# Kernel tuning notes

Hardware: AMD Instinct MI355X
Metric: run time of the kernel (lower is better)

## Reference

```python
import jax, jax.numpy as jnp
import numpy as np

LN_EPS = 1e-5


def setup_inputs() -> dict:
    key = jax.random.key(0)
    ks = jax.random.split(key, 9)
    B, S, D = 8, 2048, 512
    scale = 1.0 / np.sqrt(D)
    inp = {
        "z_q": jax.random.normal(ks[0], (B, S, D), jnp.float32),
        "z_k": jax.random.normal(ks[1], (B, S, D), jnp.float32),
        "z_v": jax.random.normal(ks[2], (B, S, D), jnp.float32),
        "Wq": jax.random.normal(ks[3], (D, D), jnp.float32) * scale,
        "bq": jnp.zeros((D,), jnp.float32),
        "Wk": jax.random.normal(ks[4], (D, D), jnp.float32) * scale,
        "bk": jnp.zeros((D,), jnp.float32),
        "Wv": jax.random.normal(ks[5], (D, D), jnp.float32) * scale,
        "bv": jnp.zeros((D,), jnp.float32),
        "ln_gamma": jnp.ones((D,), jnp.float32),
        "ln_beta": jnp.zeros((D,), jnp.float32),
    }
    return inp


def reference(z_q, z_k, z_v, Wq, bq, Wk, bk, Wv, bv, ln_gamma, ln_beta):
    # Linear projections (torch Linear: x @ W^T + b)
    Q = jnp.einsum("bsd,ed->bse", z_q, Wq) + bq  # [B, Sq, D]
    K = jnp.einsum("bsd,ed->bse", z_k, Wk) + bk  # [B, Sk, D]
    V = jnp.einsum("bsd,ed->bse", z_v, Wv) + bv  # [B, Sk, D]

    d = K.shape[-1]
    scores = jnp.einsum("bqd,bkd->bqk", Q, K) / jnp.sqrt(jnp.float32(d))
    attn = jax.nn.softmax(scores, axis=-1)  # [B, Sq, Sk]
    z_fused = jnp.einsum("bqk,bkd->bqd", attn, V)

    # LayerNorm over last dim
    mu = jnp.mean(z_fused, axis=-1, keepdims=True)
    var = jnp.var(z_fused, axis=-1, keepdims=True)
    z_norm = (z_fused - mu) * jax.lax.rsqrt(var + LN_EPS)
    return z_norm * ln_gamma + ln_beta
```

## Files before the change

kernel.cpp:

```cpp
#include <hip/hip_runtime.h>

typedef short v8s __attribute__((ext_vector_type(8)));
typedef float v4f __attribute__((ext_vector_type(4)));
typedef unsigned short u16;

#define SCALE_QK 0.04419417382415922f
#define ATTN_LDS (131072 + 17408 + 8192 + 256)

static __device__ __forceinline__ u16 f2bf(float f){
  unsigned u = __float_as_uint(f);
  u += 0x7fffu + ((u >> 16) & 1u);
  return (u16)(u >> 16);
}

static __device__ __forceinline__ void gload16(const void* g, void* l){
  __builtin_amdgcn_global_load_lds(
      (const __attribute__((address_space(1))) unsigned int*)(g),
      (__attribute__((address_space(3))) unsigned int*)(l), 16, 0, 0);
}

static __device__ __forceinline__ void bar_pub(){
  asm volatile("s_waitcnt lgkmcnt(0)" ::: "memory");
  __builtin_amdgcn_s_barrier();
  asm volatile("" ::: "memory");
}

template<int WA, int WB, int RF, int CF>
static __device__ __forceinline__ void proj_body(
    const float* __restrict__ A, const float* __restrict__ Bm,
    const float* __restrict__ bias, bool biasA, float oscale,
    u16* __restrict__ O, size_t ldo, int a0, int b0, char* sm)
{
  constexpr int AR = WA*RF*16;
  constexpr int BR = WB*CF*16;
  char* SA = sm;
  char* SB = sm + AR*64;
  const int t = threadIdx.x;
  const int l = t & 63, lm = l & 15, lg = l >> 4;
  const int w = t >> 6;
  const int wa = w / WB, wb = w % WB;
  const int swz = (lm & 3) << 4;

  v4f acc[RF][CF];
  #pragma unroll
  for (int i=0;i<RF;i++)
    #pragma unroll
    for (int j=0;j<CF;j++) acc[i][j] = (v4f){0.f,0.f,0.f,0.f};

  const int quad = t & 3;
  for (int kt=0; kt<16; ++kt){
    __syncthreads();
    #pragma unroll
    for (int rr0 = 0; rr0 < AR; rr0 += 128){
      int rr = rr0 + (t >> 2);
      const float* g = A + (size_t)(a0+rr)*512 + kt*32 + quad*8;
      float4 x0 = *(const float4*)g;
      float4 x1 = *(const float4*)(g+4);
      int4 pk;
      pk.x = (int)((unsigned)f2bf(x0.x) | ((unsigned)f2bf(x0.y)<<16));
      pk.y = (int)((unsigned)f2bf(x0.z) | ((unsigned)f2bf(x0.w)<<16));
      pk.z = (int)((unsigned)f2bf(x1.x) | ((unsigned)f2bf(x1.y)<<16));
      pk.w = (int)((unsigned)f2bf(x1.z) | ((unsigned)f2bf(x1.w)<<16));
      *(int4*)(SA + rr*64 + ((quad*16) ^ ((rr&3)<<4))) = pk;
    }
    #pragma unroll
    for (int rr0 = 0; rr0 < BR; rr0 += 128){
      int rr = rr0 + (t >> 2);
      const float* g = Bm + (size_t)(b0+rr)*512 + kt*32 + quad*8;
      float4 x0 = *(const float4*)g;
      float4 x1 = *(const float4*)(g+4);
      int4 pk;
      pk.x = (int)((unsigned)f2bf(x0.x) | ((unsigned)f2bf(x0.y)<<16));
      pk.y = (int)((unsigned)f2bf(x0.z) | ((unsigned)f2bf(x0.w)<<16));
      pk.z = (int)((unsigned)f2bf(x1.x) | ((unsigned)f2bf(x1.y)<<16));
      pk.w = (int)((unsigned)f2bf(x1.z) | ((unsigned)f2bf(x1.w)<<16));
      *(int4*)(SB + rr*64 + ((quad*16) ^ ((rr&3)<<4))) = pk;
    }
    __syncthreads();
    v8s af[RF], bf[CF];
    #pragma unroll
    for (int mf=0; mf<RF; ++mf)
      af[mf] = *(const v8s*)(SA + (wa*RF*16 + mf*16 + lm)*64 + ((lg*16) ^ swz));
    #pragma unroll
    for (int nf=0; nf<CF; ++nf)
      bf[nf] = *(const v8s*)(SB + (wb*CF*16 + nf*16 + lm)*64 + ((lg*16) ^ swz));
    #pragma unroll
    for (int mf=0; mf<RF; ++mf)
      #pragma unroll
      for (int nf=0; nf<CF; ++nf)
        acc[mf][nf] = __builtin_amdgcn_mfma_f32_16x16x32_bf16(af[mf], bf[nf], acc[mf][nf], 0, 0, 0);
  }

  float bb[CF];
  if (!biasA){
    #pragma unroll
    for (int nf=0;nf<CF;nf++) bb[nf] = bias[b0 + wb*CF*16 + nf*16 + lm];
  }
  #pragma unroll
  for (int mf=0; mf<RF; ++mf){
    #pragma unroll
    for (int r=0;r<4;r++){
      int ar = a0 + wa*RF*16 + mf*16 + lg*4 + r;
      float ba = biasA ? bias[ar] : 0.0f;
      #pragma unroll
      for (int nf=0;nf<CF;nf++){
        int bc = b0 + wb*CF*16 + nf*16 + lm;
        float v = acc[mf][nf][r] + (biasA ? ba : bb[nf]);
        O[(size_t)ar*ldo + bc] = f2bf(v * oscale);
      }
    }
  }
}

__global__ __launch_bounds__(512, 2) void proj_kernel(
    const float* __restrict__ zq, const float* __restrict__ zk, const float* __restrict__ zv,
    const float* __restrict__ Wq, const float* __restrict__ Wk, const float* __restrict__ Wv,
    const float* __restrict__ bq, const float* __restrict__ bk, const float* __restrict__ bv,
    u16* __restrict__ Qb, u16* __restrict__ Kb, u16* __restrict__ VTb)
{
  extern __shared__ char sm[];
  const int z = blockIdx.y, bx = blockIdx.x;
  if (z == 0)      proj_body<2,4,4,8>(zq, Wq, bq, false, SCALE_QK, Qb, 512, bx*128, 0, sm);
  else if (z == 1) proj_body<2,4,4,8>(zk, Wk, bk, false, 1.0f,     Kb, 512, bx*128, 0, sm);
  else             proj_body<4,2,8,4>(Wv, zv, bv, true,  1.0f,     VTb, 16384, 0, bx*128, sm);
}

static __device__ __forceinline__ void stage_k(const u16* Kb0, int j, char* Kbuf, int w, int l){
  const u16* Kt = Kb0 + (size_t)j*64*512;
  #pragma unroll
  for (int c=0;c<8;c++){
    int r = w*8 + c;
    gload16(Kt + (size_t)r*512 + (((l*16) ^ (c<<4))>>1), Kbuf + r*1024);
  }
}
static __device__ __forceinline__ void stage_v(const u16* Vb0, int j, char* Vbuf, int w, int l){
  const u16* Vt = Vb0 + (size_t)j*64;
  #pragma unroll
  for (int c=0;c<8;c++){
    int e0 = w*64 + c*8;
    gload16(Vt + (size_t)(e0 + (l>>3))*16384 + ((((l&7)*16) ^ ((l>>3)<<4))>>1), Vbuf + e0*128);
  }
}

__global__ __launch_bounds__(512, 2) void attn_kernel(
    const u16* __restrict__ Qg, const u16* __restrict__ Kg, const u16* __restrict__ VTg,
    const float* __restrict__ gamma, const float* __restrict__ beta,
    float* __restrict__ Outg)
{
  extern __shared__ char lds[];
  char*  Kbuf = lds;
  char*  Vbuf = lds + 65536;
  float* Ss   = (float*)(lds + 131072);
  char*  Pb   = lds + 131072 + 17408;
  float* st_l = (float*)(lds + 131072 + 17408 + 8192);

  const int t = threadIdx.x;
  const int l = t & 63;
  const int lm = l & 15, lg = l >> 4;
  const int w = t >> 6;
  const int wm = w >> 2;
  const int wn = w & 3;
  const int bid = blockIdx.x;
  const int b = bid & 7;
  const int q0 = (bid >> 3) * 64;

  const u16* Qt  = Qg  + ((size_t)b*2048 + q0)*512;
  const u16* Kb0 = Kg  + (size_t)b*2048*512;
  const u16* Vb0 = VTg + (size_t)b*2048;

  v8s qf[2][16];
  #pragma unroll
  for (int mf=0; mf<2; ++mf){
    const u16* qp = Qt + (size_t)(wm*32+mf*16+lm)*512 + lg*8;
    #pragma unroll
    for (int st=0; st<16; ++st)
      qf[mf][st] = *(const v8s*)(qp + st*32);
  }

  if (t < 64) st_l[t] = 0.0f;

  v4f acc[2][8];
  #pragma unroll
  for (int i=0;i<2;i++)
    #pragma unroll
    for (int j=0;j<8;j++) acc[i][j] = (v4f){0.f,0.f,0.f,0.f};

  stage_k(Kb0, 0, Kbuf, w, l);
  asm volatile("s_waitcnt vmcnt(0)" ::: "memory");
  bar_pub();
  stage_v(Vb0, 0, Vbuf, w, l);

  #pragma unroll 1
  for (int kt=0; kt<32; ++kt){
    {
      v4f s0 = (v4f){0.f,0.f,0.f,0.f}, s1 = (v4f){0.f,0.f,0.f,0.f};
      const char* kb = Kbuf + (wn*16+lm)*1024;
      const int ksw = (lm&7)<<4;
      #pragma unroll
      for (int st=0; st<16; ++st){
        v8s bfr = *(const v8s*)(kb + ((st*64 + lg*16) ^ ksw));
        s0 = __builtin_amdgcn_mfma_f32_16x16x32_bf16(qf[0][st], bfr, s0, 0,0,0);
        s1 = __builtin_amdgcn_mfma_f32_16x16x32_bf16(qf[1][st], bfr, s1, 0,0,0);
      }
      #pragma unroll
      for (int r=0;r<4;r++){
        Ss[(wm*32 +      lg*4 + r)*68 + wn*16 + lm] = s0[r];
        Ss[(wm*32 + 16 + lg*4 + r)*68 + wn*16 + lm] = s1[r];
      }
    }
    bar_pub();
    if (kt < 31) stage_k(Kb0, kt+1, Kbuf, w, l);
    {
      const int row = t >> 3, sub = t & 7;
      const float* sp = Ss + row*68 + sub*8;
      float4 sa = *(const float4*)sp;
      float4 sb = *(const float4*)(sp+4);
      float p0=__expf(sa.x), p1=__expf(sa.y), p2=__expf(sa.z), p3=__expf(sa.w);
      float p4=__expf(sb.x), p5=__expf(sb.y), p6=__expf(sb.z), p7=__expf(sb.w);
      float ps = ((p0+p1)+(p2+p3))+((p4+p5)+(p6+p7));
      ps += __shfl_xor(ps,1);
      ps += __shfl_xor(ps,2);
      ps += __shfl_xor(ps,4);
      int4 pk;
      pk.x = (int)((unsigned)f2bf(p0) | ((unsigned)f2bf(p1)<<16));
      pk.y = (int)((unsigned)f2bf(p2) | ((unsigned)f2bf(p3)<<16));
      pk.z = (int)((unsigned)f2bf(p4) | ((unsigned)f2bf(p5)<<16));
      pk.w = (int)((unsigned)f2bf(p6) | ((unsigned)f2bf(p7)<<16));
      *(int4*)(Pb + row*128 + ((sub*16) ^ ((row&7)<<4))) = pk;
      if (sub == 0) st_l[row] += ps;
    }
    if (kt < 31) { asm volatile("s_waitcnt vmcnt(8)" ::: "memory"); }
    else         { asm volatile("s_waitcnt vmcnt(0)" ::: "memory"); }
    bar_pub();
    #pragma unroll
    for (int ks=0; ks<2; ++ks){
      const int k2 = ks*64 + lg*16;
      const int psw = (lm&7)<<4;
      v8s pa0 = *(const v8s*)(Pb + (wm*32      + lm)*128 + (k2 ^ psw));
      v8s pa1 = *(const v8s*)(Pb + (wm*32 + 16 + lm)*128 + (k2 ^ psw));
      #pragma unroll
      for (int nf=0; nf<8; ++nf){
        const int e = wn*128 + nf*16 + lm;
        v8s vb = *(const v8s*)(Vbuf + e*128 + (k2 ^ psw));
        acc[0][nf] = __builtin_amdgcn_mfma_f32_16x16x32_bf16(pa0, vb, acc[0][nf], 0,0,0);
        acc[1][nf] = __builtin_amdgcn_mfma_f32_16x16x32_bf16(pa1, vb, acc[1][nf], 0,0,0);
      }
    }
    asm volatile("s_waitcnt vmcnt(0)" ::: "memory");
    bar_pub();
    if (kt < 31) stage_v(Vb0, kt+1, Vbuf, w, l);
  }

  float gv[8], bw[8];
  #pragma unroll
  for (int nf=0;nf<8;nf++){ int col = wn*128+nf*16+lm; gv[nf]=gamma[col]; bw[nf]=beta[col]; }

  float* part = Ss;
  #pragma unroll
  for (int mf=0; mf<2; ++mf){
    #pragma unroll
    for (int r=0;r<4;r++){
      int row = wm*32 + mf*16 + lg*4 + r;
      float inv = 1.0f / st_l[row];
      float s1 = 0.f, s2 = 0.f;
      #pragma unroll
      for (int nf=0;nf<8;nf++){
        float x = acc[mf][nf][r] * inv;
        acc[mf][nf][r] = x;
        s1 += x; s2 += x*x;
      }
      s1 += __shfl_xor(s1,1); s2 += __shfl_xor(s2,1);
      s1 += __shfl_xor(s1,2); s2 += __shfl_xor(s2,2);
      s1 += __shfl_xor(s1,4); s2 += __shfl_xor(s2,4);
      s1 += __shfl_xor(s1,8); s2 += __shfl_xor(s2,8);
      if (lm == 0){
        part[row*4 + wn] = s1;
        part[256 + row*4 + wn] = s2;
      }
    }
  }
  bar_pub();
  float* st_mu = (float*)Pb;
  float* st_rs = (float*)(Pb + 256);
  if (t < 64){
    float s1 = part[t*4+0]+part[t*4+1]+part[t*4+2]+part[t*4+3];
    float s2 = part[256+t*4+0]+part[256+t*4+1]+part[256+t*4+2]+part[256+t*4+3];
    float mu = s1 * (1.0f/512.0f);
    float var = s2 * (1.0f/512.0f) - mu*mu;
    st_mu[t] = mu;
    st_rs[t] = rsqrtf(fmaxf(var, 0.0f) + 1e-5f);
  }
  bar_pub();
  float* Og = Outg + ((size_t)b*2048 + q0)*512;
  #pragma unroll
  for (int mf=0; mf<2; ++mf){
    #pragma unroll
    for (int r=0;r<4;r++){
      int row = wm*32 + mf*16 + lg*4 + r;
      float mu = st_mu[row], rs = st_rs[row];
      #pragma unroll
      for (int nf=0;nf<8;nf++){
        int col = wn*128 + nf*16 + lm;
        Og[(size_t)row*512 + col] = (acc[mf][nf][r] - mu)*rs*gv[nf] + bw[nf];
      }
    }
  }
}

extern "C" void kernel_launch(void* const* d_in, const int* in_sizes, int n_in,
                              void* d_out, int out_size, void* d_ws, size_t ws_size,
                              hipStream_t stream) {
  const float* z_q  = (const float*)d_in[0];
  const float* z_k  = (const float*)d_in[1];
  const float* z_v  = (const float*)d_in[2];
  const float* Wq   = (const float*)d_in[3];
  const float* bq   = (const float*)d_in[4];
  const float* Wk   = (const float*)d_in[5];
  const float* bk   = (const float*)d_in[6];
  const float* Wv   = (const float*)d_in[7];
  const float* bv   = (const float*)d_in[8];
  const float* gam  = (const float*)d_in[9];
  const float* bet  = (const float*)d_in[10];
  float* out = (float*)d_out;

  u16* Qb  = (u16*)d_ws;
  u16* Kb  = Qb + (size_t)16384*512;
  u16* VTb = Kb + (size_t)16384*512;

  hipFuncSetAttribute(reinterpret_cast<const void*>(&proj_kernel),
                      hipFuncAttributeMaxDynamicSharedMemorySize, 40960);
  hipFuncSetAttribute(reinterpret_cast<const void*>(&attn_kernel),
                      hipFuncAttributeMaxDynamicSharedMemorySize, ATTN_LDS);

  proj_kernel<<<dim3(128,3), 512, 40960, stream>>>(z_q, z_k, z_v, Wq, Wk, Wv, bq, bk, bv, Qb, Kb, VTb);
  attn_kernel<<<256, 512, ATTN_LDS, stream>>>(Qb, Kb, VTb, gam, bet, out);
}
```

Baseline: 461.2 us.

## Restructure attention warp tiling, double-buffer K, pre-convert weights to bf16

Weights are converted to bf16 once by a new kernel and then streamed into LDS with async global-to-LDS loads, and the projection is split into separate Q/K and V kernels. The attention kernel is retiled so that each warp owns a slice of the output columns. It double-buffers K tiles in LDS and loads V fragments straight from global memory into registers instead of staging them in LDS. The exp/rowsum is computed directly on the MFMA score registers, which removes the fp32 score scratch and one barrier per iteration. The risks are higher register pressure and uncoalesced V reads from global memory, plus an extra kernel launch.

```diff
diff --git a/kernel.cpp b/kernel.cpp
--- a/kernel.cpp
+++ b/kernel.cpp
@@ -5,124 +5,185 @@
 typedef unsigned short u16;
 
 #define SCALE_QK 0.04419417382415922f
-#define ATTN_LDS (131072 + 17408 + 8192 + 256)
+#define ATTN_LDS 145664
 
 static __device__ __forceinline__ u16 f2bf(float f){
   unsigned u = __float_as_uint(f);
   u += 0x7fffu + ((u >> 16) & 1u);
   return (u16)(u >> 16);
 }
-
+static __device__ __forceinline__ unsigned pk2(float a, float b){
+  return (unsigned)f2bf(a) | ((unsigned)f2bf(b) << 16);
+}
 static __device__ __forceinline__ void gload16(const void* g, void* l){
   __builtin_amdgcn_global_load_lds(
       (const __attribute__((address_space(1))) unsigned int*)(g),
       (__attribute__((address_space(3))) unsigned int*)(l), 16, 0, 0);
 }
-
-static __device__ __forceinline__ void bar_pub(){
+static __device__ __forceinline__ void bar_ds(){
   asm volatile("s_waitcnt lgkmcnt(0)" ::: "memory");
   __builtin_amdgcn_s_barrier();
   asm volatile("" ::: "memory");
 }
 
-template<int WA, int WB, int RF, int CF>
-static __device__ __forceinline__ void proj_body(
-    const float* __restrict__ A, const float* __restrict__ Bm,
-    const float* __restrict__ bias, bool biasA, float oscale,
-    u16* __restrict__ O, size_t ldo, int a0, int b0, char* sm)
+__global__ __launch_bounds__(256) void convert_w(
+    const float* __restrict__ Wq, const float* __restrict__ Wk,
+    const float* __restrict__ Wv, u16* __restrict__ Wo)
 {
-  constexpr int AR = WA*RF*16;
-  constexpr int BR = WB*CF*16;
-  char* SA = sm;
-  char* SB = sm + AR*64;
-  const int t = threadIdx.x;
-  const int l = t & 63, lm = l & 15, lg = l >> 4;
-  const int w = t >> 6;
-  const int wa = w / WB, wb = w % WB;
-  const int swz = (lm & 3) << 4;
-
-  v4f acc[RF][CF];
-  #pragma unroll
-  for (int i=0;i<RF;i++)
-    #pragma unroll
-    for (int j=0;j<CF;j++) acc[i][j] = (v4f){0.f,0.f,0.f,0.f};
-
-  const int quad = t & 3;
+  const float* src = (blockIdx.y==0) ? Wq : (blockIdx.y==1) ? Wk : Wv;
+  u16* dst = Wo + (size_t)blockIdx.y * 262144;
+  int i = blockIdx.x*256 + threadIdx.x;
+  const float4* s = (const float4*)src + (size_t)i*2;
+  float4 a = s[0], b = s[1];
+  *(ushort4*)(dst + (size_t)i*8)     = make_ushort4(f2bf(a.x),f2bf(a.y),f2bf(a.z),f2bf(a.w));
+  *(ushort4*)(dst + (size_t)i*8 + 4) = make_ushort4(f2bf(b.x),f2bf(b.y),f2bf(b.z),f2bf(b.w));
+}
+
+__global__ __launch_bounds__(512, 2) void proj_qk(
+    const float* __restrict__ zq, const float* __restrict__ zk,
+    const u16* __restrict__ Wb,
+    const float* __restrict__ bq, const float* __restrict__ bk,
+    u16* __restrict__ Qb, u16* __restrict__ Kb)
+{
+  __shared__ char SA[128*64];
+  __shared__ char SB[512*64];
+  const int y = blockIdx.y;
+  const float* Z    = y ? zk : zq;
+  const u16*  W     = Wb + (size_t)y*262144;
+  const float* bias = y ? bk : bq;
+  u16* O            = y ? Kb : Qb;
+  const float oscale = y ? 1.0f : SCALE_QK;
+
+  const int t = threadIdx.x, l = t&63, lm = l&15, lg = l>>4, w = t>>6;
+  const int wa = w>>2, wb2 = w&3;
+  const int m0 = blockIdx.x*128;
+
+  v4f acc[4][8];
+  #pragma unroll
+  for (int i=0;i<4;i++)
+    #pragma unroll
+    for (int j=0;j<8;j++) acc[i][j] = (v4f){0.f,0.f,0.f,0.f};
+
+  const int arow = t>>2, aq = t&3;
+  #pragma unroll 1
   for (int kt=0; kt<16; ++kt){
     __syncthreads();
-    #pragma unroll
-    for (int rr0 = 0; rr0 < AR; rr0 += 128){
-      int rr = rr0 + (t >> 2);
-      const float* g = A + (size_t)(a0+rr)*512 + kt*32 + quad*8;
+    {
+      const float* g = Z + (size_t)(m0+arow)*512 + kt*32 + aq*8;
       float4 x0 = *(const float4*)g;
       float4 x1 = *(const float4*)(g+4);
-      int4 pk;
-      pk.x = (int)((unsigned)f2bf(x0.x) | ((unsigned)f2bf(x0.y)<<16));
-      pk.y = (int)((unsigned)f2bf(x0.z) | ((unsigned)f2bf(x0.w)<<16));
-      pk.z = (int)((unsigned)f2bf(x1.x) | ((unsigned)f2bf(x1.y)<<16));
-      pk.w = (int)((unsigned)f2bf(x1.z) | ((unsigned)f2bf(x1.w)<<16));
-      *(int4*)(SA + rr*64 + ((quad*16) ^ ((rr&3)<<4))) = pk;
-    }
-    #pragma unroll
-    for (int rr0 = 0; rr0 < BR; rr0 += 128){
-      int rr = rr0 + (t >> 2);
-      const float* g = Bm + (size_t)(b0+rr)*512 + kt*32 + quad*8;
+      int4 pk = { (int)pk2(x0.x,x0.y), (int)pk2(x0.z,x0.w),
+                  (int)pk2(x1.x,x1.y), (int)pk2(x1.z,x1.w) };
+      *(int4*)(SA + arow*64 + ((aq*16) ^ ((arow&3)<<4))) = pk;
+    }
+    #pragma unroll
+    for (int i=0;i<4;i++){
+      int rbase = i*128 + w*16;
+      int r = rbase + (l>>2), c = l&3;
+      gload16(W + (size_t)r*512 + kt*32 + ((c ^ (r&3))*8), SB + rbase*64);
+    }
+    __syncthreads();
+    v8s af[4], bf[8];
+    #pragma unroll
+    for (int mf=0; mf<4; ++mf){
+      int m = wa*64 + mf*16 + lm;
+      af[mf] = *(const v8s*)(SA + m*64 + ((lg*16) ^ ((m&3)<<4)));
+    }
+    #pragma unroll
+    for (int nf=0; nf<8; ++nf){
+      int n = wb2*128 + nf*16 + lm;
+      bf[nf] = *(const v8s*)(SB + n*64 + ((lg*16) ^ ((n&3)<<4)));
+    }
+    #pragma unroll
+    for (int mf=0; mf<4; ++mf)
+      #pragma unroll
+      for (int nf=0; nf<8; ++nf)
+        acc[mf][nf] = __builtin_amdgcn_mfma_f32_16x16x32_bf16(af[mf], bf[nf], acc[mf][nf], 0,0,0);
+  }
+
+  float bb[8];
+  #pragma unroll
+  for (int nf=0;nf<8;nf++) bb[nf] = bias[wb2*128 + nf*16 + lm];
+  #pragma unroll
+  for (int mf=0; mf<4; ++mf){
+    #pragma unroll
+    for (int r=0;r<4;r++){
+      int m = m0 + wa*64 + mf*16 + lg*4 + r;
+      #pragma unroll
+      for (int nf=0;nf<8;nf++){
+        int n = wb2*128 + nf*16 + lm;
+        O[(size_t)m*512 + n] = f2bf((acc[mf][nf][r] + bb[nf]) * oscale);
+      }
+    }
+  }
+}
+
+__global__ __launch_bounds__(512, 2) void proj_v(
+    const float* __restrict__ zv, const u16* __restrict__ Wvb,
+    const float* __restrict__ bv, u16* __restrict__ VTb)
+{
+  __shared__ char SA[512*64];
+  __shared__ char SB[128*64];
+  const int t = threadIdx.x, l = t&63, lm = l&15, lg = l>>4, w = t>>6;
+  const int wn = w>>1, wm2 = w&1;
+  const int m0 = blockIdx.x*128;
+
+  v4f acc[8][4];
+  #pragma unroll
+  for (int i=0;i<8;i++)
+    #pragma unroll
+    for (int j=0;j<4;j++) acc[i][j] = (v4f){0.f,0.f,0.f,0.f};
+
+  const int brow = t>>2, bq2 = t&3;
+  #pragma unroll 1
+  for (int kt=0; kt<16; ++kt){
+    __syncthreads();
+    {
+      const float* g = zv + (size_t)(m0+brow)*512 + kt*32 + bq2*8;
       float4 x0 = *(const float4*)g;
       float4 x1 = *(const float4*)(g+4);
-      int4 pk;
-      pk.x = (int)((unsigned)f2bf(x0.x) | ((unsigned)f2bf(x0.y)<<16));
-      pk.y = (int)((unsigned)f2bf(x0.z) | ((unsigned)f2bf(x0.w)<<16));
-      pk.z = (int)((unsigned)f2bf(x1.x) | ((unsigned)f2bf(x1.y)<<16));
-      pk.w = (int)((unsigned)f2bf(x1.z) | ((unsigned)f2bf(x1.w)<<16));
-      *(int4*)(SB + rr*64 + ((quad*16) ^ ((rr&3)<<4))) = pk;
+      int4 pk = { (int)pk2(x0.x,x0.y), (int)pk2(x0.z,x0.w),
+                  (int)pk2(x1.x,x1.y), (int)pk2(x1.z,x1.w) };
+      *(int4*)(SB + brow*64 + ((bq2*16) ^ ((brow&3)<<4))) = pk;
+    }
+    #pragma unroll
+    for (int i=0;i<4;i++){
+      int rbase = i*128 + w*16;
+      int r = rbase + (l>>2), c = l&3;
+      gload16(Wvb + (size_t)r*512 + kt*32 + ((c ^ (r&3))*8), SA + rbase*64);
     }
     __syncthreads();
-    v8s af[RF], bf[CF];
-    #pragma unroll
-    for (int mf=0; mf<RF; ++mf)
-      af[mf] = *(const v8s*)(SA + (wa*RF*16 + mf*16 + lm)*64 + ((lg*16) ^ swz));
-    #pragma unroll
-    for (int nf=0; nf<CF; ++nf)
-      bf[nf] = *(const v8s*)(SB + (wb*CF*16 + nf*16 + lm)*64 + ((lg*16) ^ swz));
-    #pragma unroll
-    for (int mf=0; mf<RF; ++mf)
-      #pragma unroll
-      for (int nf=0; nf<CF; ++nf)
-        acc[mf][nf] = __builtin_amdgcn_mfma_f32_16x16x32_bf16(af[mf], bf[nf], acc[mf][nf], 0, 0, 0);
-  }
-
-  float bb[CF];
-  if (!biasA){
-    #pragma unroll
-    for (int nf=0;nf<CF;nf++) bb[nf] = bias[b0 + wb*CF*16 + nf*16 + lm];
-  }
-  #pragma unroll
-  for (int mf=0; mf<RF; ++mf){
+    v8s af[8], bf[4];
+    #pragma unroll
+    for (int mf=0; mf<8; ++mf){
+      int n = wn*128 + mf*16 + lm;
+      af[mf] = *(const v8s*)(SA + n*64 + ((lg*16) ^ ((n&3)<<4)));
+    }
+    #pragma unroll
+    for (int nf=0; nf<4; ++nf){
+      int m = wm2*64 + nf*16 + lm;
+      bf[nf] = *(const v8s*)(SB + m*64 + ((lg*16) ^ ((m&3)<<4)));
+    }
+    #pragma unroll
+    for (int mf=0; mf<8; ++mf)
+      #pragma unroll
+      for (int nf=0; nf<4; ++nf)
+        acc[mf][nf] = __builtin_amdgcn_mfma_f32_16x16x32_bf16(af[mf], bf[nf], acc[mf][nf], 0,0,0);
+  }
+
+  #pragma unroll
+  for (int mf=0; mf<8; ++mf){
     #pragma unroll
     for (int r=0;r<4;r++){
-      int ar = a0 + wa*RF*16 + mf*16 + lg*4 + r;
-      float ba = biasA ? bias[ar] : 0.0f;
-      #pragma unroll
-      for (int nf=0;nf<CF;nf++){
-        int bc = b0 + wb*CF*16 + nf*16 + lm;
-        float v = acc[mf][nf][r] + (biasA ? ba : bb[nf]);
-        O[(size_t)ar*ldo + bc] = f2bf(v * oscale);
-      }
-    }
-  }
-}
-
-__global__ __launch_bounds__(512, 2) void proj_kernel(
-    const float* __restrict__ zq, const float* __restrict__ zk, const float* __restrict__ zv,
-    const float* __restrict__ Wq, const float* __restrict__ Wk, const float* __restrict__ Wv,
-    const float* __restrict__ bq, const float* __restrict__ bk, const float* __restrict__ bv,
-    u16* __restrict__ Qb, u16* __restrict__ Kb, u16* __restrict__ VTb)
-{
-  extern __shared__ char sm[];
-  const int z = blockIdx.y, bx = blockIdx.x;
-  if (z == 0)      proj_body<2,4,4,8>(zq, Wq, bq, false, SCALE_QK, Qb, 512, bx*128, 0, sm);
-  else if (z == 1) proj_body<2,4,4,8>(zk, Wk, bk, false, 1.0f,     Kb, 512, bx*128, 0, sm);
-  else             proj_body<4,2,8,4>(Wv, zv, bv, true,  1.0f,     VTb, 16384, 0, bx*128, sm);
+      int n = wn*128 + mf*16 + lg*4 + r;
+      float ba = bv[n];
+      #pragma unroll
+      for (int nf=0;nf<4;nf++){
+        int m = m0 + wm2*64 + nf*16 + lm;
+        VTb[(size_t)n*16384 + m] = f2bf(acc[mf][nf][r] + ba);
+      }
+    }
+  }
 }
 
 static __device__ __forceinline__ void stage_k(const u16* Kb0, int j, char* Kbuf, int w, int l){
@@ -131,14 +192,6 @@
   for (int c=0;c<8;c++){
     int r = w*8 + c;
     gload16(Kt + (size_t)r*512 + (((l*16) ^ (c<<4))>>1), Kbuf + r*1024);
-  }
-}
-static __device__ __forceinline__ void stage_v(const u16* Vb0, int j, char* Vbuf, int w, int l){
-  const u16* Vt = Vb0 + (size_t)j*64;
-  #pragma unroll
-  for (int c=0;c<8;c++){
-    int e0 = w*64 + c*8;
-    gload16(Vt + (size_t)(e0 + (l>>3))*16384 + ((((l&7)*16) ^ ((l>>3)<<4))>>1), Vbuf + e0*128);
   }
 }
 
@@ -148,21 +201,17 @@
     float* __restrict__ Outg)
 {
   extern __shared__ char lds[];
-  char*  Kbuf = lds;
-  char*  Vbuf = lds + 65536;
-  float* Ss   = (float*)(lds + 131072);
-  char*  Pb   = lds + 131072 + 17408;
-  float* st_l = (float*)(lds + 131072 + 17408 + 8192);
-
-  const int t = threadIdx.x;
-  const int l = t & 63;
-  const int lm = l & 15, lg = l >> 4;
-  const int w = t >> 6;
-  const int wm = w >> 2;
-  const int wn = w & 3;
-  const int bid = blockIdx.x;
-  const int b = bid & 7;
-  const int q0 = (bid >> 3) * 64;
+  char*  Pb    = lds + 131072;
+  float* part  = (float*)(lds + 139264);
+  float* st_l  = (float*)(lds + 140288);
+  float* part2 = (float*)(lds + 140544);
+  float* st_mu = (float*)(lds + 145152);
+  float* st_rs = (float*)(lds + 145408);
+
+  const int t = threadIdx.x, l = t&63, lm = l&15, lg = l>>4, w = t>>6;
+  const int wq = w&1, wk = w>>1;
+  const int wd = w;
+  const int bid = blockIdx.x, b = bid&7, q0 = (bid>>3)*64;
 
   const u16* Qt  = Qg  + ((size_t)b*2048 + q0)*512;
   const u16* Kb0 = Kg  + (size_t)b*2048*512;
@@ -170,102 +219,100 @@
 
   v8s qf[2][16];
   #pragma unroll
-  for (int mf=0; mf<2; ++mf){
-    const u16* qp = Qt + (size_t)(wm*32+mf*16+lm)*512 + lg*8;
+  for (int f=0; f<2; ++f){
+    const u16* qp = Qt + (size_t)(wq*32+f*16+lm)*512 + lg*8;
     #pragma unroll
     for (int st=0; st<16; ++st)
-      qf[mf][st] = *(const v8s*)(qp + st*32);
+      qf[f][st] = *(const v8s*)(qp + st*32);
   }
 
   if (t < 64) st_l[t] = 0.0f;
 
-  v4f acc[2][8];
-  #pragma unroll
-  for (int i=0;i<2;i++)
-    #pragma unroll
-    for (int j=0;j<8;j++) acc[i][j] = (v4f){0.f,0.f,0.f,0.f};
-
-  stage_k(Kb0, 0, Kbuf, w, l);
+  v4f acc[4][4];
+  #pragma unroll
+  for (int i=0;i<4;i++)
+    #pragma unroll
+    for (int j=0;j<4;j++) acc[i][j] = (v4f){0.f,0.f,0.f,0.f};
+
+  stage_k(Kb0, 0, lds, w, l);
   asm volatile("s_waitcnt vmcnt(0)" ::: "memory");
-  bar_pub();
-  stage_v(Vb0, 0, Vbuf, w, l);
-
+  bar_ds();
+
+  const int vrow = wd*64 + lm;
   #pragma unroll 1
   for (int kt=0; kt<32; ++kt){
+    char* kb_cur = lds + ((kt&1)<<16);
+    char* kb_nxt = lds + (((kt+1)&1)<<16);
+    const u16* Vk = Vb0 + (size_t)kt*64;
+
+    v8s vf0[4], vf1[4];
+    #pragma unroll
+    for (int nf=0; nf<4; ++nf)
+      vf0[nf] = *(const v8s*)(Vk + (size_t)(vrow + nf*16)*16384 + lg*8);
+    #pragma unroll
+    for (int nf=0; nf<4; ++nf)
+      vf1[nf] = *(const v8s*)(Vk + (size_t)(vrow + nf*16)*16384 + 32 + lg*8);
+    if (kt < 31) stage_k(Kb0, kt+1, kb_nxt, w, l);
+
+    v4f s0 = (v4f){0.f,0.f,0.f,0.f}, s1 = (v4f){0.f,0.f,0.f,0.f};
     {
-      v4f s0 = (v4f){0.f,0.f,0.f,0.f}, s1 = (v4f){0.f,0.f,0.f,0.f};
-      const char* kb = Kbuf + (wn*16+lm)*1024;
+      const char* krow = kb_cur + (size_t)(wk*16+lm)*1024;
       const int ksw = (lm&7)<<4;
       #pragma unroll
       for (int st=0; st<16; ++st){
-        v8s bfr = *(const v8s*)(kb + ((st*64 + lg*16) ^ ksw));
-        s0 = __builtin_amdgcn_mfma_f32_16x16x32_bf16(qf[0][st], bfr, s0, 0,0,0);
-        s1 = __builtin_amdgcn_mfma_f32_16x16x32_bf16(qf[1][st], bfr, s1, 0,0,0);
-      }
-      #pragma unroll
-      for (int r=0;r<4;r++){
-        Ss[(wm*32 +      lg*4 + r)*68 + wn*16 + lm] = s0[r];
-        Ss[(wm*32 + 16 + lg*4 + r)*68 + wn*16 + lm] = s1[r];
-      }
-    }
-    bar_pub();
-    if (kt < 31) stage_k(Kb0, kt+1, Kbuf, w, l);
+        v8s kf = *(const v8s*)(krow + ((st*64 + lg*16) ^ ksw));
+        s0 = __builtin_amdgcn_mfma_f32_16x16x32_bf16(kf, qf[0][st], s0, 0,0,0);
+        s1 = __builtin_amdgcn_mfma_f32_16x16x32_bf16(kf, qf[1][st], s1, 0,0,0);
+      }
+    }
+    float p00=__expf(s0[0]), p01=__expf(s0[1]), p02=__expf(s0[2]), p03=__expf(s0[3]);
+    float p10=__expf(s1[0]), p11=__expf(s1[1]), p12=__expf(s1[2]), p13=__expf(s1[3]);
+    float ps0 = (p00+p01)+(p02+p03);
+    float ps1 = (p10+p11)+(p12+p13);
+    ps0 += __shfl_xor(ps0,16); ps0 += __shfl_xor(ps0,32);
+    ps1 += __shfl_xor(ps1,16); ps1 += __shfl_xor(ps1,32);
+    if (l < 16){
+      part[(wq*32 +      lm)*4 + wk] = ps0;
+      part[(wq*32 + 16 + lm)*4 + wk] = ps1;
+    }
     {
-      const int row = t >> 3, sub = t & 7;
-      const float* sp = Ss + row*68 + sub*8;
-      float4 sa = *(const float4*)sp;
-      float4 sb = *(const float4*)(sp+4);
-      float p0=__expf(sa.x), p1=__expf(sa.y), p2=__expf(sa.z), p3=__expf(sa.w);
-      float p4=__expf(sb.x), p5=__expf(sb.y), p6=__expf(sb.z), p7=__expf(sb.w);
-      float ps = ((p0+p1)+(p2+p3))+((p4+p5)+(p6+p7));
-      ps += __shfl_xor(ps,1);
-      ps += __shfl_xor(ps,2);
-      ps += __shfl_xor(ps,4);
-      int4 pk;
-      pk.x = (int)((unsigned)f2bf(p0) | ((unsigned)f2bf(p1)<<16));
-      pk.y = (int)((unsigned)f2bf(p2) | ((unsigned)f2bf(p3)<<16));
-      pk.z = (int)((unsigned)f2bf(p4) | ((unsigned)f2bf(p5)<<16));
-      pk.w = (int)((unsigned)f2bf(p6) | ((unsigned)f2bf(p7)<<16));
-      *(int4*)(Pb + row*128 + ((sub*16) ^ ((row&7)<<4))) = pk;
-      if (sub == 0) st_l[row] += ps;
-    }
-    if (kt < 31) { asm volatile("s_waitcnt vmcnt(8)" ::: "memory"); }
-    else         { asm volatile("s_waitcnt vmcnt(0)" ::: "memory"); }
-    bar_pub();
-    #pragma unroll
-    for (int ks=0; ks<2; ++ks){
-      const int k2 = ks*64 + lg*16;
-      const int psw = (lm&7)<<4;
-      v8s pa0 = *(const v8s*)(Pb + (wm*32      + lm)*128 + (k2 ^ psw));
-      v8s pa1 = *(const v8s*)(Pb + (wm*32 + 16 + lm)*128 + (k2 ^ psw));
-      #pragma unroll
-      for (int nf=0; nf<8; ++nf){
-        const int e = wn*128 + nf*16 + lm;
-        v8s vb = *(const v8s*)(Vbuf + e*128 + (k2 ^ psw));
-        acc[0][nf] = __builtin_amdgcn_mfma_f32_16x16x32_bf16(pa0, vb, acc[0][nf], 0,0,0);
-        acc[1][nf] = __builtin_amdgcn_mfma_f32_16x16x32_bf16(pa1, vb, acc[1][nf], 0,0,0);
+      int qa = wq*32 + lm, qb = wq*32 + 16 + lm;
+      int cix = wk*2 + (lg>>1), half = (lg&1)*8;
+      *(int2*)(Pb + qa*128 + ((cix ^ (qa&7))<<4) + half) =
+          make_int2((int)pk2(p00,p01), (int)pk2(p02,p03));
+      *(int2*)(Pb + qb*128 + ((cix ^ (qb&7))<<4) + half) =
+          make_int2((int)pk2(p10,p11), (int)pk2(p12,p13));
+    }
+
+    bar_ds();
+
+    if (t < 64) st_l[t] += part[t*4+0]+part[t*4+1]+part[t*4+2]+part[t*4+3];
+
+    #pragma unroll
+    for (int mf=0; mf<4; ++mf){
+      int qq = mf*16 + lm;
+      v8s pa0 = *(const v8s*)(Pb + qq*128 + ((lg       ^ (qq&7))<<4));
+      v8s pa1 = *(const v8s*)(Pb + qq*128 + (((4 + lg) ^ (qq&7))<<4));
+      #pragma unroll
+      for (int nf=0; nf<4; ++nf){
+        acc[mf][nf] = __builtin_amdgcn_mfma_f32_16x16x32_bf16(pa0, vf0[nf], acc[mf][nf], 0,0,0);
+        acc[mf][nf] = __builtin_amdgcn_mfma_f32_16x16x32_bf16(pa1, vf1[nf], acc[mf][nf], 0,0,0);
       }
     }
     asm volatile("s_waitcnt vmcnt(0)" ::: "memory");
-    bar_pub();
-    if (kt < 31) stage_v(Vb0, kt+1, Vbuf, w, l);
-  }
-
-  float gv[8], bw[8];
-  #pragma unroll
-  for (int nf=0;nf<8;nf++){ int col = wn*128+nf*16+lm; gv[nf]=gamma[col]; bw[nf]=beta[col]; }
-
-  float* part = Ss;
-  #pragma unroll
-  for (int mf=0; mf<2; ++mf){
+    bar_ds();
+  }
+
+  #pragma unroll
+  for (int mf=0; mf<4; ++mf){
     #pragma unroll
     for (int r=0;r<4;r++){
-      int row = wm*32 + mf*16 + lg*4 + r;
-      float inv = 1.0f / st_l[row];
+      int qq = mf*16 + lg*4 + r;
+      float il = 1.0f / st_l[qq];
       float s1 = 0.f, s2 = 0.f;
       #pragma unroll
-      for (int nf=0;nf<8;nf++){
-        float x = acc[mf][nf][r] * inv;
+      for (int nf=0;nf<4;nf++){
+        float x = acc[mf][nf][r] * il;
         acc[mf][nf][r] = x;
         s1 += x; s2 += x*x;
       }
@@ -274,34 +321,35 @@
       s1 += __shfl_xor(s1,4); s2 += __shfl_xor(s2,4);
       s1 += __shfl_xor(s1,8); s2 += __shfl_xor(s2,8);
       if (lm == 0){
-        part[row*4 + wn] = s1;
-        part[256 + row*4 + wn] = s2;
-      }
-    }
-  }
-  bar_pub();
-  float* st_mu = (float*)Pb;
-  float* st_rs = (float*)(Pb + 256);
+        part2[qq*9 + wd] = s1;
+        part2[576 + qq*9 + wd] = s2;
+      }
+    }
+  }
+  bar_ds();
   if (t < 64){
-    float s1 = part[t*4+0]+part[t*4+1]+part[t*4+2]+part[t*4+3];
-    float s2 = part[256+t*4+0]+part[256+t*4+1]+part[256+t*4+2]+part[256+t*4+3];
-    float mu = s1 * (1.0f/512.0f);
-    float var = s2 * (1.0f/512.0f) - mu*mu;
+    float a = 0.f, c = 0.f;
+    #pragma unroll
+    for (int j=0;j<8;j++){ a += part2[t*9+j]; c += part2[576 + t*9+j]; }
+    float mu = a * (1.0f/512.0f);
+    float var = c * (1.0f/512.0f) - mu*mu;
     st_mu[t] = mu;
     st_rs[t] = rsqrtf(fmaxf(var, 0.0f) + 1e-5f);
   }
-  bar_pub();
+  bar_ds();
+  float gv[4], bw[4];
+  #pragma unroll
+  for (int nf=0;nf<4;nf++){ int col = wd*64+nf*16+lm; gv[nf]=gamma[col]; bw[nf]=beta[col]; }
   float* Og = Outg + ((size_t)b*2048 + q0)*512;
   #pragma unroll
-  for (int mf=0; mf<2; ++mf){
+  for (int mf=0; mf<4; ++mf){
     #pragma unroll
     for (int r=0;r<4;r++){
-      int row = wm*32 + mf*16 + lg*4 + r;
-      float mu = st_mu[row], rs = st_rs[row];
-      #pragma unroll
-      for (int nf=0;nf<8;nf++){
-        int col = wn*128 + nf*16 + lm;
-        Og[(size_t)row*512 + col] = (acc[mf][nf][r] - mu)*rs*gv[nf] + bw[nf];
+      int qq = mf*16 + lg*4 + r;
+      float mu = st_mu[qq], rs = st_rs[qq];
+      #pragma unroll
+      for (int nf=0;nf<4;nf++){
+        Og[(size_t)qq*512 + wd*64 + nf*16 + lm] = (acc[mf][nf][r] - mu)*rs*gv[nf] + bw[nf];
       }
     }
   }
@@ -326,12 +374,13 @@
   u16* Qb  = (u16*)d_ws;
   u16* Kb  = Qb + (size_t)16384*512;
   u16* VTb = Kb + (size_t)16384*512;
-
-  hipFuncSetAttribute(reinterpret_cast<const void*>(&proj_kernel),
-                      hipFuncAttributeMaxDynamicSharedMemorySize, 40960);
+  u16* Wb  = VTb + (size_t)16384*512;
+
   hipFuncSetAttribute(reinterpret_cast<const void*>(&attn_kernel),
                       hipFuncAttributeMaxDynamicSharedMemorySize, ATTN_LDS);
 
-  proj_kernel<<<dim3(128,3), 512, 40960, stream>>>(z_q, z_k, z_v, Wq, Wk, Wv, bq, bk, bv, Qb, Kb, VTb);
+  convert_w<<<dim3(128,3), 256, 0, stream>>>(Wq, Wk, Wv, Wb);
+  proj_qk<<<dim3(128,2), 512, 0, stream>>>(z_q, z_k, Wb, bq, bk, Qb, Kb);
+  proj_v<<<128, 512, 0, stream>>>(z_v, Wb + (size_t)2*262144, bv, VTb);
   attn_kernel<<<256, 512, ATTN_LDS, stream>>>(Qb, Kb, VTb, gam, bet, out);
 }
```

New measurement: 469.0 us. No clear change (+1.7%).
